# Performance work log

Measured on AMD Instinct MI355X. Metric: run time of the kernel, lower is better.

Reference implementation:

```python
import jax, jax.numpy as jnp
import numpy as np

T, L, C = 256, 32, 8
B, D = 16, 512


def _content_matrix(T, L, C):
    # Faithful port of compute_content_matrix: binary indicator (L, L, C, T).
    # Only upper-triangular (i <= j) window pairs are populated.
    Wc = np.zeros((L, L, C, T), dtype=np.float32)
    stride = T // L
    for i in range(L):
        for j in range(i, L):
            window_size = j - i + 1
            window_start = i * stride
            num_frames = window_size * stride
            clip_size = num_frames // C if num_frames > C else 1
            for c in range(min(C, num_frames)):
                clip_start = window_start + c * clip_size
                Wc[i, j, c, clip_start:clip_start + clip_size] = 1.0
    return Wc


def setup_inputs() -> dict:
    key = jax.random.key(0)
    f = jax.random.normal(key, (B, T, D), dtype=jnp.float32)
    Wc = jnp.asarray(_content_matrix(T, L, C))
    return {"f": f, "Wc": Wc}


def reference(f, Wc):
    # fc[b,l,m,c,d] = sum_t Wc[l,m,c,t] * f[b,t,d]  -> clip content features
    fc = jnp.einsum('lmct,btd->blmcd', Wc, f)  # (B, L, L, C, D)
    # fm: sum over clips within each window
    fm = jnp.sum(fc, axis=3)  # (B, L, L, D)
    # NOTE: original torch code overwrites the avg-pooled tensor with a fresh
    # permute of f, so fb is just f transposed (the pooling result is discarded).
    fb = jnp.transpose(f, (0, 2, 1))  # (B, D, T)
    return fc, fm, fb
```

## Files before the change

### kernel.cpp

```cpp
#include <hip/hip_runtime.h>

#define TT 256
#define LL 32
#define CC 8
#define BB 16
#define DD 512
#define D4 (DD / 4)

#define FC_ELEMS ((long)BB * LL * LL * CC * DD)
#define FM_ELEMS ((long)BB * LL * LL * DD)
#define FM_OFF   FC_ELEMS
#define FB_OFF   (FC_ELEMS + FM_ELEMS)

#define S_ROWS   (TT + 1)

#define SCHUNK   8
#define NSCHUNK  (TT / SCHUNK)
#define D4PB     8

__device__ __forceinline__ float4 f4add(float4 a, float4 b) {
  return make_float4(a.x + b.x, a.y + b.y, a.z + b.z, a.w + b.w);
}
__device__ __forceinline__ float4 f4sub(float4 a, float4 b) {
  return make_float4(a.x - b.x, a.y - b.y, a.z - b.z, a.w - b.w);
}

typedef float nf4 __attribute__((ext_vector_type(4)));
__device__ __forceinline__ void ntstore(float4* p, float4 v) {
  nf4 nv;
  nv.x = v.x; nv.y = v.y; nv.z = v.z; nv.w = v.w;
  __builtin_nontemporal_store(nv, (nf4*)p);
}

__global__ __launch_bounds__(256) void scan_fb_kernel(
    const float4* __restrict__ f4, float4* __restrict__ S4,
    float4* __restrict__ fb4) {
  __shared__ float4 part[NSCHUNK][D4PB];

  int b = blockIdx.x >> 4;
  int d4blk = blockIdx.x & 15;
  int d4local = threadIdx.x & (D4PB - 1);
  int chunk = threadIdx.x >> 3;
  int d4 = d4blk * D4PB + d4local;

  const float4* fp = f4 + ((long)(b * TT + chunk * SCHUNK)) * D4 + d4;
  float4 vals[SCHUNK];
  float4 s = make_float4(0.f, 0.f, 0.f, 0.f);
#pragma unroll
  for (int i = 0; i < SCHUNK; ++i) {
    vals[i] = fp[(long)i * D4];
    s = f4add(s, vals[i]);
  }
  part[chunk][d4local] = s;
  __syncthreads();

  float4 acc = make_float4(0.f, 0.f, 0.f, 0.f);
  for (int j = 0; j < chunk; ++j) acc = f4add(acc, part[j][d4local]);

  float4* Sp = S4 + ((long)b * S_ROWS + chunk * SCHUNK) * D4 + d4;
  if (chunk == 0) Sp[0] = make_float4(0.f, 0.f, 0.f, 0.f);
#pragma unroll
  for (int i = 0; i < SCHUNK; ++i) {
    acc = f4add(acc, vals[i]);
    Sp[(long)(i + 1) * D4] = acc;
  }

  const float* v = (const float*)vals;
#pragma unroll
  for (int dd = 0; dd < 4; ++dd) {
    float4* fbp = fb4 + (long)(b * DD + 4 * d4 + dd) * (TT / 4) + chunk * 2;
#pragma unroll
    for (int j = 0; j < 2; ++j) {
      float4 t = make_float4(v[(4 * j + 0) * 4 + dd], v[(4 * j + 1) * 4 + dd],
                             v[(4 * j + 2) * 4 + dd], v[(4 * j + 3) * 4 + dd]);
      ntstore(&fbp[j], t);
    }
  }
}

__global__ __launch_bounds__(128) void fc_fm_kernel(
    const float* __restrict__ S, float* __restrict__ out) {
  int i = blockIdx.x;
  int vblk = ((i & 7) << 11) | (i >> 3);
  int b = vblk >> 10;
  int l = (vblk >> 5) & (LL - 1);
  int m = vblk & (LL - 1);
  int d4 = threadIdx.x;

  float4* outv = (float4*)out;
  long blm = (long)((b * LL + l) * LL + m);
  long fc_base = blm * CC * D4;
  long fm_base = FM_OFF / 4 + blm * D4;

  if (l > m) {
    float4 z = make_float4(0.f, 0.f, 0.f, 0.f);
#pragma unroll
    for (int c = 0; c < CC; ++c) ntstore(&outv[fc_base + (long)c * D4 + d4], z);
    ntstore(&outv[fm_base + d4], z);
    return;
  }

  int w = m - l + 1;
  const float4* S4 = (const float4*)S;
  long srow = (long)b * S_ROWS;

  float4 s[9];
#pragma unroll
  for (int c = 0; c <= 8; ++c) {
    int p = 8 * l + c * w;
    s[c] = S4[(srow + p) * D4 + d4];
  }

#pragma unroll
  for (int c = 0; c < CC; ++c)
    ntstore(&outv[fc_base + (long)c * D4 + d4], f4sub(s[c + 1], s[c]));
  ntstore(&outv[fm_base + d4], f4sub(s[8], s[0]));
}

extern "C" void kernel_launch(void* const* d_in, const int* in_sizes, int n_in,
                              void* d_out, int out_size, void* d_ws, size_t ws_size,
                              hipStream_t stream) {
  const float4* f4 = (const float4*)d_in[0];
  float* out = (float*)d_out;

  float4* S4 = (float4*)d_ws;
  float4* fb4 = (float4*)(out + FB_OFF);

  scan_fb_kernel<<<BB * (D4 / D4PB), 256, 0, stream>>>(f4, S4, fb4);
  fc_fm_kernel<<<BB * LL * LL, 128, 0, stream>>>((const float*)S4, out);
}
```

Baseline: 319.1 us.

## Fuse prefix-scan and fc/fm output into one kernel using LDS prefix sums

Merges the scan/transpose kernel and the fc/fm writer into a single kernel. Each block computes the prefix sums for a batch and an 8-float4 slice of D into shared memory, then writes half of the (l,m,c) outputs from LDS. This removes the global workspace round-trip and one launch. In exchange, each block has fewer parallel lanes on d, uses higher LDS per block, and issues more fragmented 128-byte store segments.

```diff
diff --git a/kernel.cpp b/kernel.cpp
--- a/kernel.cpp
+++ b/kernel.cpp
@@ -12,11 +12,11 @@
 #define FM_OFF   FC_ELEMS
 #define FB_OFF   (FC_ELEMS + FM_ELEMS)
 
-#define S_ROWS   (TT + 1)
-
 #define SCHUNK   8
-#define NSCHUNK  (TT / SCHUNK)
-#define D4PB     8
+#define NCH      (TT / SCHUNK)
+#define GD4      8
+#define NG       (D4 / GD4)
+#define SPAD     9
 
 __device__ __forceinline__ float4 f4add(float4 a, float4 b) {
   return make_float4(a.x + b.x, a.y + b.y, a.z + b.z, a.w + b.w);
@@ -32,16 +32,20 @@
   __builtin_nontemporal_store(nv, (nf4*)p);
 }
 
-__global__ __launch_bounds__(256) void scan_fb_kernel(
-    const float4* __restrict__ f4, float4* __restrict__ S4,
-    float4* __restrict__ fb4) {
-  __shared__ float4 part[NSCHUNK][D4PB];
+__global__ __launch_bounds__(256) void fused_kernel(
+    const float4* __restrict__ f4, float* __restrict__ out) {
+  __shared__ float4 Sl[TT + 1][SPAD];
+  __shared__ float4 part[NCH][GD4];
 
-  int b = blockIdx.x >> 4;
-  int d4blk = blockIdx.x & 15;
-  int d4local = threadIdx.x & (D4PB - 1);
-  int chunk = threadIdx.x >> 3;
-  int d4 = d4blk * D4PB + d4local;
+  int bid = blockIdx.x;
+  int half = bid & 1;
+  int g = (bid >> 1) & (NG - 1);
+  int b = bid >> 5;
+
+  int tid = threadIdx.x;
+  int d4l = tid & (GD4 - 1);
+  int chunk = tid >> 3;
+  int d4 = g * GD4 + d4l;
 
   const float4* fp = f4 + ((long)(b * TT + chunk * SCHUNK)) * D4 + d4;
   float4 vals[SCHUNK];
@@ -51,70 +55,68 @@
     vals[i] = fp[(long)i * D4];
     s = f4add(s, vals[i]);
   }
-  part[chunk][d4local] = s;
+  part[chunk][d4l] = s;
   __syncthreads();
 
   float4 acc = make_float4(0.f, 0.f, 0.f, 0.f);
-  for (int j = 0; j < chunk; ++j) acc = f4add(acc, part[j][d4local]);
+  for (int j = 0; j < chunk; ++j) acc = f4add(acc, part[j][d4l]);
 
-  float4* Sp = S4 + ((long)b * S_ROWS + chunk * SCHUNK) * D4 + d4;
-  if (chunk == 0) Sp[0] = make_float4(0.f, 0.f, 0.f, 0.f);
+  if (chunk == 0) Sl[0][d4l] = make_float4(0.f, 0.f, 0.f, 0.f);
 #pragma unroll
   for (int i = 0; i < SCHUNK; ++i) {
     acc = f4add(acc, vals[i]);
-    Sp[(long)(i + 1) * D4] = acc;
+    Sl[chunk * SCHUNK + 1 + i][d4l] = acc;
   }
 
-  const float* v = (const float*)vals;
+  if (half == 0) {
+    float4* fb4 = (float4*)(out + FB_OFF);
+    const float* v = (const float*)vals;
 #pragma unroll
-  for (int dd = 0; dd < 4; ++dd) {
-    float4* fbp = fb4 + (long)(b * DD + 4 * d4 + dd) * (TT / 4) + chunk * 2;
+    for (int dd = 0; dd < 4; ++dd) {
+      float4* fbp = fb4 + (long)(b * DD + 4 * d4 + dd) * (TT / 4) + chunk * 2;
 #pragma unroll
-    for (int j = 0; j < 2; ++j) {
-      float4 t = make_float4(v[(4 * j + 0) * 4 + dd], v[(4 * j + 1) * 4 + dd],
-                             v[(4 * j + 2) * 4 + dd], v[(4 * j + 3) * 4 + dd]);
-      ntstore(&fbp[j], t);
+      for (int j = 0; j < 2; ++j) {
+        ntstore(&fbp[j],
+                make_float4(v[(4 * j + 0) * 4 + dd], v[(4 * j + 1) * 4 + dd],
+                            v[(4 * j + 2) * 4 + dd], v[(4 * j + 3) * 4 + dd]));
+      }
     }
   }
-}
-
-__global__ __launch_bounds__(128) void fc_fm_kernel(
-    const float* __restrict__ S, float* __restrict__ out) {
-  int i = blockIdx.x;
-  int vblk = ((i & 7) << 11) | (i >> 3);
-  int b = vblk >> 10;
-  int l = (vblk >> 5) & (LL - 1);
-  int m = vblk & (LL - 1);
-  int d4 = threadIdx.x;
+  __syncthreads();
 
   float4* outv = (float4*)out;
-  long blm = (long)((b * LL + l) * LL + m);
-  long fc_base = blm * CC * D4;
-  long fm_base = FM_OFF / 4 + blm * D4;
+  int cs = chunk;
+  int lmbase = half << 9;
 
-  if (l > m) {
-    float4 z = make_float4(0.f, 0.f, 0.f, 0.f);
-#pragma unroll
-    for (int c = 0; c < CC; ++c) ntstore(&outv[fc_base + (long)c * D4 + d4], z);
-    ntstore(&outv[fm_base + d4], z);
-    return;
+  for (int it = 0; it < 128; ++it) {
+    int gc = it * 32 + cs;
+    int lm = lmbase + (gc >> 3);
+    int c = gc & 7;
+    int l = lm >> 5, m = lm & 31;
+    float4 vv;
+    if (l <= m) {
+      int w = m - l + 1;
+      int p0 = 8 * l + c * w;
+      vv = f4sub(Sl[p0 + w][d4l], Sl[p0][d4l]);
+    } else {
+      vv = make_float4(0.f, 0.f, 0.f, 0.f);
+    }
+    long off = ((long)(b * 1024 + lm)) * 1024 + c * 128 + d4;
+    ntstore(&outv[off], vv);
   }
 
-  int w = m - l + 1;
-  const float4* S4 = (const float4*)S;
-  long srow = (long)b * S_ROWS;
-
-  float4 s[9];
-#pragma unroll
-  for (int c = 0; c <= 8; ++c) {
-    int p = 8 * l + c * w;
-    s[c] = S4[(srow + p) * D4 + d4];
+  for (int it = 0; it < 16; ++it) {
+    int lm = lmbase + it * 32 + cs;
+    int l = lm >> 5, m = lm & 31;
+    float4 vv;
+    if (l <= m) {
+      vv = f4sub(Sl[8 * (m + 1)][d4l], Sl[8 * l][d4l]);
+    } else {
+      vv = make_float4(0.f, 0.f, 0.f, 0.f);
+    }
+    long off = FM_OFF / 4 + ((long)(b * 1024 + lm)) * 128 + d4;
+    ntstore(&outv[off], vv);
   }
-
-#pragma unroll
-  for (int c = 0; c < CC; ++c)
-    ntstore(&outv[fc_base + (long)c * D4 + d4], f4sub(s[c + 1], s[c]));
-  ntstore(&outv[fm_base + d4], f4sub(s[8], s[0]));
 }
 
 extern "C" void kernel_launch(void* const* d_in, const int* in_sizes, int n_in,
@@ -123,9 +125,5 @@
   const float4* f4 = (const float4*)d_in[0];
   float* out = (float*)d_out;
 
-  float4* S4 = (float4*)d_ws;
-  float4* fb4 = (float4*)(out + FB_OFF);
-
-  scan_fb_kernel<<<BB * (D4 / D4PB), 256, 0, stream>>>(f4, S4, fb4);
-  fc_fm_kernel<<<BB * LL * LL, 128, 0, stream>>>((const float*)S4, out);
+  fused_kernel<<<BB * NG * 2, 256, 0, stream>>>(f4, out);
 }
```

Measured after the change: 328.2 us. 2.9% more time.
